# Kernel optimization log

Measured on AMD Instinct MI355X. Metric: run time of the kernel, lower is better.

## Reference

```python
import jax, jax.numpy as jnp
import numpy as np

N, F_IN, H, C, E = 50000, 128, 4, 32, 800000
NEG_SLOPE = 0.2


def setup_inputs() -> dict:
    key = jax.random.key(0)
    ks = jax.random.split(key, 6)
    x = jax.random.normal(ks[0], (N, F_IN), dtype=jnp.float32)
    edge_index = jax.random.randint(ks[1], (2, E), 0, N, dtype=jnp.int64)
    scale = 1.0 / np.sqrt(F_IN)
    Wl = jax.random.normal(ks[2], (F_IN, H * C), dtype=jnp.float32) * scale
    Wr = jax.random.normal(ks[3], (F_IN, H * C), dtype=jnp.float32) * scale
    att = jax.random.normal(ks[4], (H, C), dtype=jnp.float32) * (1.0 / np.sqrt(C))
    bias = jax.random.normal(ks[5], (H * C,), dtype=jnp.float32) * 0.01
    return {"x": x, "edge_index": edge_index, "Wl": Wl, "Wr": Wr, "att": att, "bias": bias}


def reference(x, edge_index, Wl, Wr, att, bias):
    n = x.shape[0]
    # add self loops (add_self_loops=True, edge_dim=None)
    loop = jnp.arange(n, dtype=edge_index.dtype)
    ei = jnp.concatenate([edge_index, jnp.stack([loop, loop])], axis=1)
    src, dst = ei[0], ei[1]  # messages flow src -> dst; softmax over dst
    # share_weights=False: separate projections for source (l) and target (r)
    xl = (x @ Wl).reshape(n, H, C)
    xr = (x @ Wr).reshape(n, H, C)
    # GATv2 edge score: a . LeakyReLU(xl[src] + xr[dst])
    e = xl[src] + xr[dst]                      # [Et, H, C]
    e = jnp.where(e > 0, e, NEG_SLOPE * e)
    logits = jnp.einsum('ehc,hc->eh', e, att)  # [Et, H]
    # segment softmax over destination nodes (every node has a self loop)
    m = jax.ops.segment_max(logits, dst, num_segments=n)
    ex = jnp.exp(logits - m[dst])
    den = jax.ops.segment_sum(ex, dst, num_segments=n)
    alpha = ex / den[dst]                      # [Et, H]
    # weighted scatter-aggregate of source messages
    out = jax.ops.segment_sum(alpha[:, :, None] * xl[src], dst, num_segments=n)
    out = out.reshape(n, H * C) + bias         # concat=True heads, bias
    out = jax.nn.relu(out)                     # activation_func='relu'
    return out, alpha
```

## Files before the change

kernel.cpp:

```cpp
#include <hip/hip_runtime.h>
#include <hip/hip_bf16.h>
#include <hip/hip_fp16.h>

#define F_IN   128
#define HC     128
#define NH     4
#define NEG_SLOPE 0.2f
#define CAP2   48
#define NBUCK  196
#define EBLK   4096

typedef __attribute__((ext_vector_type(8))) short short8;
typedef __attribute__((ext_vector_type(4))) float f32x4;
typedef _Float16 h2 __attribute__((ext_vector_type(2)));

__device__ __forceinline__ unsigned short f2bf(float f) {
    union { float f; unsigned u; } c; c.f = f;
    unsigned u = c.u;
    u += 0x7FFFu + ((u >> 16) & 1u);
    return (unsigned short)(u >> 16);
}

__device__ __forceinline__ float fdot2f(h2 a, h2 b, float c) {
#if __has_builtin(__builtin_amdgcn_fdot2)
    return __builtin_amdgcn_fdot2(a, b, c, false);
#else
    return fmaf((float)a[0], (float)b[0], fmaf((float)a[1], (float)b[1], c));
#endif
}

union U4H { uint4 u; h2 h[4]; };

__global__ __launch_bounds__(1024) void wpack_split_kernel(
    const float* __restrict__ Wl, const float* __restrict__ Wr,
    short* __restrict__ BlP, short* __restrict__ BrP,
    const int* __restrict__ ei,
    int2* __restrict__ bucketRec,
    unsigned short* __restrict__ offT,
    int E)
{
    __shared__ int  hist[256];
    __shared__ int  sc[256];
    __shared__ int2 stage[EBLK];
    const int t = threadIdx.x;

    if ((int)blockIdx.x < 4) {
        const int tid = (int)blockIdx.x * 1024 + t;
        const int mat = tid >> 11;
        const int r   = tid & 2047;
        const int f   = r >> 6;
        const int l   = r & 63;
        const int tt  = f & 3;
        const int ct  = f >> 2;
        const int kb  = tt * 32 + (l >> 4) * 8;
        const int c   = ct * 16 + (l & 15);
        const float* W = mat ? Wr : Wl;
        short*       P = mat ? BrP : BlP;
        short8 v;
        #pragma unroll
        for (int j = 0; j < 8; ++j)
            v[j] = (short)f2bf(W[(size_t)(kb + j) * HC + c]);
        *(short8*)&P[(size_t)(f * 64 + l) * 8] = v;
        return;
    }

    const int sb = (int)blockIdx.x - 4;
    const int e0 = sb * EBLK;

    if (t < 256) hist[t] = 0;
    __syncthreads();

    int dsts[4], srcs[4], rk[4];
    #pragma unroll
    for (int k = 0; k < 4; ++k) {
        const int e = e0 + k * 1024 + t;
        dsts[k] = (e < E) ? ei[E + e] : -1;
        srcs[k] = (e < E) ? ei[e] : 0;
    }
    #pragma unroll
    for (int k = 0; k < 4; ++k)
        rk[k] = (dsts[k] >= 0) ? atomicAdd(&hist[dsts[k] >> 8], 1) : 0;
    __syncthreads();

    if (t < 256) sc[t] = hist[t];
    __syncthreads();
    for (int off = 1; off < 256; off <<= 1) {
        int v = 0, u = 0;
        if (t < 256) { v = sc[t]; u = (t >= off) ? sc[t - off] : 0; }
        __syncthreads();
        if (t < 256) sc[t] = v + u;
        __syncthreads();
    }
    if (t < NBUCK)
        offT[(size_t)sb * NBUCK + t] = (unsigned short)(sc[t] - hist[t]);

    #pragma unroll
    for (int k = 0; k < 4; ++k) {
        if (dsts[k] >= 0) {
            const int e    = e0 + k * 1024 + t;
            const int bkt  = dsts[k] >> 8;
            const int base = sc[bkt] - hist[bkt];
            stage[base + rk[k]] =
                make_int2(e | ((dsts[k] & 255) << 24), srcs[k]);
        }
    }
    __syncthreads();

    const int4* st4 = (const int4*)stage;
    int4* g4 = (int4*)(bucketRec + (size_t)sb * EBLK);
    g4[t]        = st4[t];
    g4[t + 1024] = st4[t + 1024];
}

__global__ __launch_bounds__(1024) void proj_gather_kernel(
    const float* __restrict__ x,
    const short* __restrict__ BlP,
    const short* __restrict__ BrP,
    unsigned short* __restrict__ xlb,
    unsigned short* __restrict__ xrb,
    const int2* __restrict__ bucketRec,
    const unsigned short* __restrict__ offT,
    int2* __restrict__ slot,
    int* __restrict__ cnt,
    int n, int E, int PB, int SB)
{
    __shared__ int sCnt[256];
    __shared__ int sOff[256];
    __shared__ int sI[256];
    __shared__ int cur[256];
    const int t = threadIdx.x;

    if ((int)blockIdx.x >= PB) {
        const int b = (int)blockIdx.x - PB;

        if (t < 256) {
            cur[t] = 0;
            int c = 0, o = 0;
            if (t < SB) {
                const int tot = min(EBLK, E - t * EBLK);
                o = offT[(size_t)t * NBUCK + b];
                const int o1 = (b < NBUCK - 1) ? (int)offT[(size_t)t * NBUCK + b + 1] : tot;
                c = o1 - o;
            }
            sCnt[t] = c; sOff[t] = o; sI[t] = c;
        }
        __syncthreads();
        for (int off = 1; off < 256; off <<= 1) {
            int v = 0, u = 0;
            if (t < 256) { v = sI[t]; u = (t >= off) ? sI[t - off] : 0; }
            __syncthreads();
            if (t < 256) sI[t] = v + u;
            __syncthreads();
        }
        const int cntB = sI[255];

        for (int i = t; i < cntB; i += 1024) {
            int lo = 0, hi = SB - 1;
            while (lo < hi) {
                const int mid = (lo + hi) >> 1;
                if (sI[mid] > i) hi = mid; else lo = mid + 1;
            }
            const int sb    = lo;
            const int local = i - (sI[sb] - sCnt[sb]);
            const int2 rec  = bucketRec[(size_t)sb * EBLK + sOff[sb] + local];
            const int dl  = (unsigned)rec.x >> 24;
            const int r   = atomicAdd(&cur[dl], 1);
            const int dst = (b << 8) + dl;
            if (r < CAP2)
                slot[(size_t)dst * CAP2 + r] = make_int2(rec.x & 0xFFFFFF, rec.y);
        }
        __syncthreads();
        if (t < 256) {
            const int dstT = (b << 8) + t;
            if (dstT < n) cnt[dstT] = cur[t];
        }
        return;
    }

    const int w    = t >> 6;
    const int lane = t & 63;
    const int r0   = blockIdx.x * 256 + w * 16;
    if (r0 >= n) return;
    const int q    = lane >> 4;
    const int row  = r0 + (lane & 15);

    short8 af[4];
    {
        const float* xp = x + (size_t)row * F_IN + q * 8;
        #pragma unroll
        for (int s = 0; s < 4; ++s) {
            const float4 u0 = *(const float4*)(xp + s * 32);
            const float4 u1 = *(const float4*)(xp + s * 32 + 4);
            short8 a;
            a[0] = (short)f2bf(u0.x); a[1] = (short)f2bf(u0.y);
            a[2] = (short)f2bf(u0.z); a[3] = (short)f2bf(u0.w);
            a[4] = (short)f2bf(u1.x); a[5] = (short)f2bf(u1.y);
            a[6] = (short)f2bf(u1.z); a[7] = (short)f2bf(u1.w);
            af[s] = a;
        }
    }

    f32x4 accL[8], accR[8];
    const f32x4 zero = {0.f, 0.f, 0.f, 0.f};
    #pragma unroll
    for (int ct = 0; ct < 8; ++ct) { accL[ct] = zero; accR[ct] = zero; }

    #pragma unroll
    for (int s = 0; s < 4; ++s) {
        #pragma unroll
        for (int ct = 0; ct < 8; ++ct) {
            const short8 bl = *(const short8*)&BlP[(size_t)((ct * 4 + s) * 64 + lane) * 8];
            const short8 br = *(const short8*)&BrP[(size_t)((ct * 4 + s) * 64 + lane) * 8];
            accL[ct] = __builtin_amdgcn_mfma_f32_16x16x32_bf16(af[s], bl, accL[ct], 0, 0, 0);
            accR[ct] = __builtin_amdgcn_mfma_f32_16x16x32_bf16(af[s], br, accR[ct], 0, 0, 0);
        }
    }

    const int cb = lane & 15;
    const bool evenLane = (cb & 1) == 0;
    unsigned* xl_u = (unsigned*)xlb;
    unsigned* xr_u = (unsigned*)xrb;
    #pragma unroll
    for (int ct = 0; ct < 8; ++ct) {
        #pragma unroll
        for (int i = 0; i < 4; ++i) {
            const float l = accL[ct][i];
            const float r = accR[ct][i];
            const float sl = __shfl_xor(l, 1);
            const float sr = __shfl_xor(r, 1);
            const int rowo = r0 + q * 4 + i;
            const size_t cidx = (size_t)rowo * 64 + ct * 8 + (cb >> 1);
            union { _Float16 h[2]; unsigned u; } ph;
            if (evenLane) { ph.h[0] = (_Float16)l;  ph.h[1] = (_Float16)sl; xl_u[cidx] = ph.u; }
            else          { ph.h[0] = (_Float16)sr; ph.h[1] = (_Float16)r;  xr_u[cidx] = ph.u; }
        }
    }
}

__global__ __launch_bounds__(256) void fused_agg_kernel(
    const int2* __restrict__ slot,
    const int* __restrict__ cnt,
    const unsigned short* __restrict__ xlb,
    const unsigned short* __restrict__ xrb,
    const float* __restrict__ att,
    const float* __restrict__ bias,
    float* __restrict__ alpha_out,
    float* __restrict__ out,
    int n, int E)
{
    __shared__ float lds_ex[4][256];
    const int w    = threadIdx.x >> 6;
    const int lane = threadIdx.x & 63;
    const int dst  = blockIdx.x * 4 + w;
    if (dst >= n) return;

    const int deg   = min(cnt[dst], CAP2);
    const int total = deg + 1;
    const int g     = lane >> 4;
    const int i     = lane & 15;
    const int h     = i >> 2;

    const char* xlB = (const char*)xlb;

    h2 xr2[4], at2[4];
    {
        U4H c; c.u = ((const uint4*)xrb)[(size_t)dst * 16 + i];
        xr2[0] = c.h[0]; xr2[1] = c.h[1]; xr2[2] = c.h[2]; xr2[3] = c.h[3];
        const float4 a01 = *(const float4*)&att[8 * i];
        const float4 a23 = *(const float4*)&att[8 * i + 4];
        at2[0] = h2{(_Float16)a01.x, (_Float16)a01.y};
        at2[1] = h2{(_Float16)a01.z, (_Float16)a01.w};
        at2[2] = h2{(_Float16)a23.x, (_Float16)a23.y};
        at2[3] = h2{(_Float16)a23.z, (_Float16)a23.w};
    }
    const h2 slope2 = {(_Float16)NEG_SLOPE, (_Float16)NEG_SLOPE};

    int eReg = E + dst, srcReg = dst;
    if (lane < deg) { const int2 es = slot[(size_t)dst * CAP2 + lane]; eReg = es.x; srcReg = es.y; }

    float* exrow = lds_ex[w];

    float dh = 0.f;
    float acc[8];
    #pragma unroll
    for (int k = 0; k < 8; ++k) acc[k] = 0.f;

    {
        const unsigned ib = (unsigned)i << 4;
        #define XLOAD(s) (*(const uint4*)(xlB + (((unsigned)(s) << 8) + ib)))

        const int s0 = __shfl(srcReg, g);
        uint4 u = XLOAD(s0);
        uint4 u1 = u, u2 = u, u3 = u;
        if (4 < total)  u1 = XLOAD(__shfl(srcReg, min(g + 4, 63)));
        if (8 < total)  u2 = XLOAD(__shfl(srcReg, min(g + 8, 63)));
        if (12 < total) u3 = XLOAD(__shfl(srcReg, min(g + 12, 63)));

        for (int j = 0; j < total; j += 4) {
            const int jj = j + g;
            uint4 u4 = u3;
            if (j + 16 < total) {
                const int sn = __shfl(srcReg, min(jj + 16, 63));
                u4 = XLOAD(sn);
            }

            U4H cu; cu.u = u;
            float p = 0.f;
            float vf[8];
            #pragma unroll
            for (int k = 0; k < 4; ++k) {
                const h2 v2 = cu.h[k];
                const h2 t2 = v2 + xr2[k];
                const h2 l2 = __builtin_elementwise_max(t2, t2 * slope2);
                p = fdot2f(l2, at2[k], p);
                vf[2 * k]     = (float)v2[0];
                vf[2 * k + 1] = (float)v2[1];
            }
            p += __shfl_xor(p, 1);
            p += __shfl_xor(p, 2);

            const float ex = (jj <= deg) ? __expf(p) : 0.f;
            dh += ex;
            #pragma unroll
            for (int k = 0; k < 8; ++k) acc[k] = fmaf(ex, vf[k], acc[k]);

            if ((lane & 3) == 0 && jj <= deg) exrow[jj * 4 + h] = ex;
            u = u1; u1 = u2; u2 = u3; u3 = u4;
        }
        #undef XLOAD
    }

    dh += __shfl_xor(dh, 16);
    dh += __shfl_xor(dh, 32);
    #pragma unroll
    for (int k = 0; k < 8; ++k) {
        acc[k] += __shfl_xor(acc[k], 16);
        acc[k] += __shfl_xor(acc[k], 32);
    }
    const float invh = 1.f / dh;
    const float id0 = 1.f / __shfl(dh, 0);
    const float id1 = 1.f / __shfl(dh, 4);
    const float id2 = 1.f / __shfl(dh, 8);
    const float id3 = 1.f / __shfl(dh, 12);

    __threadfence_block();

    if (lane < total) {
        const float4 e4 = *(const float4*)&exrow[lane * 4];
        const float4 a4 = make_float4(e4.x * id0, e4.y * id1, e4.z * id2, e4.w * id3);
        *(float4*)&alpha_out[(size_t)eReg * NH] = a4;
    }

    if (g == 0) {
        const float4 b01 = *(const float4*)&bias[8 * i];
        const float4 b23 = *(const float4*)&bias[8 * i + 4];
        float4 o01, o23;
        o01.x = fmaxf(fmaf(acc[0], invh, b01.x), 0.f);
        o01.y = fmaxf(fmaf(acc[1], invh, b01.y), 0.f);
        o01.z = fmaxf(fmaf(acc[2], invh, b01.z), 0.f);
        o01.w = fmaxf(fmaf(acc[3], invh, b01.w), 0.f);
        o23.x = fmaxf(fmaf(acc[4], invh, b23.x), 0.f);
        o23.y = fmaxf(fmaf(acc[5], invh, b23.y), 0.f);
        o23.z = fmaxf(fmaf(acc[6], invh, b23.z), 0.f);
        o23.w = fmaxf(fmaf(acc[7], invh, b23.w), 0.f);
        *(float4*)&out[(size_t)dst * HC + 8 * i]     = o01;
        *(float4*)&out[(size_t)dst * HC + 8 * i + 4] = o23;
    }
}

extern "C" void kernel_launch(void* const* d_in, const int* in_sizes, int n_in,
                              void* d_out, int out_size, void* d_ws, size_t ws_size,
                              hipStream_t stream)
{
    const float* x    = (const float*)d_in[0];
    const int*   ei   = (const int*)d_in[1];
    const float* Wl   = (const float*)d_in[2];
    const float* Wr   = (const float*)d_in[3];
    const float* att  = (const float*)d_in[4];
    const float* bias = (const float*)d_in[5];

    const int n  = in_sizes[0] / F_IN;
    const int E  = in_sizes[1] / 2;

    float* out   = (float*)d_out;
    float* alpha = (float*)d_out + (size_t)n * HC;

    const int SB = (E + EBLK - 1) / EBLK;
    const int PB = (n + 255) / 256;
    const int NB = (n + 255) >> 8;

    short*          BlP       = (short*)d_ws;
    short*          BrP       = BlP + 16384;
    unsigned short* xlb       = (unsigned short*)(BrP + 16384);
    unsigned short* xrb       = xlb + (size_t)n * HC;
    int2*           slot      = (int2*)(xrb + (size_t)n * HC);
    int*            cnt       = (int*)(slot + (size_t)n * CAP2);
    int2*           bucketRec = (int2*)(cnt + ((n + 3) & ~3));
    unsigned short* offT      = (unsigned short*)(bucketRec + (size_t)SB * EBLK);

    wpack_split_kernel<<<dim3(4 + SB), 1024, 0, stream>>>(
        Wl, Wr, BlP, BrP, ei, bucketRec, offT, E);

    proj_gather_kernel<<<dim3(PB + NB), 1024, 0, stream>>>(
        x, BlP, BrP, xlb, xrb, bucketRec, offT, slot, cnt, n, E, PB, SB);

    fused_agg_kernel<<<dim3((n + 3) / 4), 256, 0, stream>>>(
        slot, cnt, xlb, xrb, att, bias, alpha, out, n, E);
}
```

Measured before the change: 157.0 us.

## Split xl/xr into head-pair halves and aggregate each half in separate blocks

The projection output is stored as two planar halves (heads 0-1 and heads 2-3), each row 128 bytes instead of 256. The aggregation kernel launches twice as many blocks, and each block handles one half for a destination node. Each gathered source row is now a single 128-byte segment, which should make the random gathers more cache-friendly and give more parallelism. The cost is that the slot and count metadata are read twice, there are extra shuffle reductions, and the alpha stores are split into two half-width writes.

```diff
diff --git a/kernel.cpp b/kernel.cpp
--- a/kernel.cpp
+++ b/kernel.cpp
@@ -220,6 +220,7 @@
     const bool evenLane = (cb & 1) == 0;
     unsigned* xl_u = (unsigned*)xlb;
     unsigned* xr_u = (unsigned*)xrb;
+    const size_t halfStride = (size_t)n * 32;
     #pragma unroll
     for (int ct = 0; ct < 8; ++ct) {
         #pragma unroll
@@ -229,7 +230,8 @@
             const float sl = __shfl_xor(l, 1);
             const float sr = __shfl_xor(r, 1);
             const int rowo = r0 + q * 4 + i;
-            const size_t cidx = (size_t)rowo * 64 + ct * 8 + (cb >> 1);
+            const size_t cidx = (size_t)(ct >> 2) * halfStride
+                              + (size_t)rowo * 32 + (ct & 3) * 8 + (cb >> 1);
             union { _Float16 h[2]; unsigned u; } ph;
             if (evenLane) { ph.h[0] = (_Float16)l;  ph.h[1] = (_Float16)sl; xl_u[cidx] = ph.u; }
             else          { ph.h[0] = (_Float16)sr; ph.h[1] = (_Float16)r;  xr_u[cidx] = ph.u; }
@@ -246,28 +248,30 @@
     const float* __restrict__ bias,
     float* __restrict__ alpha_out,
     float* __restrict__ out,
-    int n, int E)
+    int n, int E, int nb2)
 {
-    __shared__ float lds_ex[4][256];
+    __shared__ float lds_ex[4][128];
+    const int half = ((int)blockIdx.x >= nb2) ? 1 : 0;
+    const int bidx = (int)blockIdx.x - (half ? nb2 : 0);
     const int w    = threadIdx.x >> 6;
     const int lane = threadIdx.x & 63;
-    const int dst  = blockIdx.x * 4 + w;
+    const int dst  = bidx * 4 + w;
     if (dst >= n) return;
 
     const int deg   = min(cnt[dst], CAP2);
     const int total = deg + 1;
-    const int g     = lane >> 4;
-    const int i     = lane & 15;
-    const int h     = i >> 2;
-
-    const char* xlB = (const char*)xlb;
+    const int g     = lane >> 3;
+    const int i     = lane & 7;
+    const int hl    = i >> 2;
+
+    const char* xlB = (const char*)xlb + (size_t)half * n * 128;
 
     h2 xr2[4], at2[4];
     {
-        U4H c; c.u = ((const uint4*)xrb)[(size_t)dst * 16 + i];
+        U4H c; c.u = ((const uint4*)xrb)[(size_t)half * n * 8 + (size_t)dst * 8 + i];
         xr2[0] = c.h[0]; xr2[1] = c.h[1]; xr2[2] = c.h[2]; xr2[3] = c.h[3];
-        const float4 a01 = *(const float4*)&att[8 * i];
-        const float4 a23 = *(const float4*)&att[8 * i + 4];
+        const float4 a01 = *(const float4*)&att[half * 64 + 8 * i];
+        const float4 a23 = *(const float4*)&att[half * 64 + 8 * i + 4];
         at2[0] = h2{(_Float16)a01.x, (_Float16)a01.y};
         at2[1] = h2{(_Float16)a01.z, (_Float16)a01.w};
         at2[2] = h2{(_Float16)a23.x, (_Float16)a23.y};
@@ -287,21 +291,18 @@
 
     {
         const unsigned ib = (unsigned)i << 4;
-        #define XLOAD(s) (*(const uint4*)(xlB + (((unsigned)(s) << 8) + ib)))
-
-        const int s0 = __shfl(srcReg, g);
-        uint4 u = XLOAD(s0);
-        uint4 u1 = u, u2 = u, u3 = u;
-        if (4 < total)  u1 = XLOAD(__shfl(srcReg, min(g + 4, 63)));
-        if (8 < total)  u2 = XLOAD(__shfl(srcReg, min(g + 8, 63)));
-        if (12 < total) u3 = XLOAD(__shfl(srcReg, min(g + 12, 63)));
-
-        for (int j = 0; j < total; j += 4) {
+        #define XLOAD(s) (*(const uint4*)(xlB + (((unsigned)(s) << 7) + ib)))
+
+        uint4 u = XLOAD(__shfl(srcReg, g));
+        uint4 u1 = u;
+        if (8 < total) u1 = XLOAD(__shfl(srcReg, min(g + 8, 63)));
+
+        for (int j = 0; j < total; j += 8) {
             const int jj = j + g;
-            uint4 u4 = u3;
+            uint4 u2 = u1;
             if (j + 16 < total) {
                 const int sn = __shfl(srcReg, min(jj + 16, 63));
-                u4 = XLOAD(sn);
+                u2 = XLOAD(sn);
             }
 
             U4H cu; cu.u = u;
@@ -324,36 +325,36 @@
             #pragma unroll
             for (int k = 0; k < 8; ++k) acc[k] = fmaf(ex, vf[k], acc[k]);
 
-            if ((lane & 3) == 0 && jj <= deg) exrow[jj * 4 + h] = ex;
-            u = u1; u1 = u2; u2 = u3; u3 = u4;
+            if ((lane & 3) == 0 && jj <= deg) exrow[jj * 2 + hl] = ex;
+            u = u1; u1 = u2;
         }
         #undef XLOAD
     }
 
+    dh += __shfl_xor(dh, 8);
     dh += __shfl_xor(dh, 16);
     dh += __shfl_xor(dh, 32);
     #pragma unroll
     for (int k = 0; k < 8; ++k) {
+        acc[k] += __shfl_xor(acc[k], 8);
         acc[k] += __shfl_xor(acc[k], 16);
         acc[k] += __shfl_xor(acc[k], 32);
     }
     const float invh = 1.f / dh;
     const float id0 = 1.f / __shfl(dh, 0);
     const float id1 = 1.f / __shfl(dh, 4);
-    const float id2 = 1.f / __shfl(dh, 8);
-    const float id3 = 1.f / __shfl(dh, 12);
 
     __threadfence_block();
 
     if (lane < total) {
-        const float4 e4 = *(const float4*)&exrow[lane * 4];
-        const float4 a4 = make_float4(e4.x * id0, e4.y * id1, e4.z * id2, e4.w * id3);
-        *(float4*)&alpha_out[(size_t)eReg * NH] = a4;
+        const float2 e2 = *(const float2*)&exrow[lane * 2];
+        const float2 a2 = make_float2(e2.x * id0, e2.y * id1);
+        *(float2*)&alpha_out[(size_t)eReg * NH + half * 2] = a2;
     }
 
     if (g == 0) {
-        const float4 b01 = *(const float4*)&bias[8 * i];
-        const float4 b23 = *(const float4*)&bias[8 * i + 4];
+        const float4 b01 = *(const float4*)&bias[half * 64 + 8 * i];
+        const float4 b23 = *(const float4*)&bias[half * 64 + 8 * i + 4];
         float4 o01, o23;
         o01.x = fmaxf(fmaf(acc[0], invh, b01.x), 0.f);
         o01.y = fmaxf(fmaf(acc[1], invh, b01.y), 0.f);
@@ -363,8 +364,8 @@
         o23.y = fmaxf(fmaf(acc[5], invh, b23.y), 0.f);
         o23.z = fmaxf(fmaf(acc[6], invh, b23.z), 0.f);
         o23.w = fmaxf(fmaf(acc[7], invh, b23.w), 0.f);
-        *(float4*)&out[(size_t)dst * HC + 8 * i]     = o01;
-        *(float4*)&out[(size_t)dst * HC + 8 * i + 4] = o23;
+        *(float4*)&out[(size_t)dst * HC + half * 64 + 8 * i]     = o01;
+        *(float4*)&out[(size_t)dst * HC + half * 64 + 8 * i + 4] = o23;
     }
 }
 
@@ -388,6 +389,7 @@
     const int SB = (E + EBLK - 1) / EBLK;
     const int PB = (n + 255) / 256;
     const int NB = (n + 255) >> 8;
+    const int nb2 = (n + 3) / 4;
 
     short*          BlP       = (short*)d_ws;
     short*          BrP       = BlP + 16384;
@@ -404,6 +406,6 @@
     proj_gather_kernel<<<dim3(PB + NB), 1024, 0, stream>>>(
         x, BlP, BrP, xlb, xrb, bucketRec, offT, slot, cnt, n, E, PB, SB);
 
-    fused_agg_kernel<<<dim3((n + 3) / 4), 256, 0, stream>>>(
-        slot, cnt, xlb, xrb, att, bias, alpha, out, n, E);
-}
+    fused_agg_kernel<<<dim3(2 * nb2), 256, 0, stream>>>(
+        slot, cnt, xlb, xrb, att, bias, alpha, out, n, E, nb2);
+}
```

Result: slower. 172.4 us (+9.8%).
